# Optimization experiments

Hardware: AMD Instinct MI355X
Metric: run time of the kernel (lower is better)

## Reference

```python
import jax, jax.numpy as jnp
import numpy as np
from jax import lax

A_RATIOS = (0.5, 1.0, 2.0)
A_SCALES = (8, 16, 32)
FEAT_STRIDE = 16
BASE_SIZE = 16
PRE_NMS = 6000     # n_test_pre_nms
POST_NMS = 300     # n_test_post_nms
NMS_THRESH = 0.7
MIN_SIZE = 16.0
SCALE = 1.0        # forward(scale=1.0) default
NEG = -1e10


def _anchor_base():
    # standard generate_anchor_base: centered at (8,8), ratios x scales
    py = px = BASE_SIZE / 2.0
    rows = []
    for r in A_RATIOS:
        for s in A_SCALES:
            h = BASE_SIZE * s * np.sqrt(r)
            w = BASE_SIZE * s * np.sqrt(1.0 / r)
            rows.append([py - h / 2.0, px - w / 2.0, py + h / 2.0, px + w / 2.0])
    return np.asarray(rows, np.float32)  # (A, 4)


def _all_anchors(height, width):
    base = jnp.asarray(_anchor_base())                                  # (A, 4)
    sy = (jnp.arange(height) * FEAT_STRIDE).astype(jnp.float32)
    sx = (jnp.arange(width) * FEAT_STRIDE).astype(jnp.float32)
    gy, gx = jnp.meshgrid(sy, sx, indexing='ij')
    shift = jnp.stack([gy.ravel(), gx.ravel(), gy.ravel(), gx.ravel()], axis=1)  # (K, 4)
    anch = base[None, :, :] + shift[:, None, :]                         # (K, A, 4)
    return anch.reshape(-1, 4)                                          # (K*A, 4)


def _conv(x, w, b, pad):
    y = lax.conv_general_dilated(x, w, (1, 1), [(pad, pad), (pad, pad)],
                                 dimension_numbers=('NCHW', 'OIHW', 'NCHW'))
    return y + b[None, :, None, None]


def _loc2bbox(anchors, locs):
    h = anchors[:, 2] - anchors[:, 0]
    w = anchors[:, 3] - anchors[:, 1]
    cy = anchors[:, 0] + 0.5 * h
    cx = anchors[:, 1] + 0.5 * w
    dy, dx, dh, dw = locs[:, 0], locs[:, 1], locs[:, 2], locs[:, 3]
    ncy = dy * h + cy
    ncx = dx * w + cx
    nh = jnp.exp(dh) * h
    nw = jnp.exp(dw) * w
    return jnp.stack([ncy - 0.5 * nh, ncx - 0.5 * nw,
                      ncy + 0.5 * nh, ncx + 0.5 * nw], axis=1)


def _iou_one_vs_all(box, boxes):
    ty = jnp.maximum(box[0], boxes[:, 0])
    tx = jnp.maximum(box[1], boxes[:, 1])
    by = jnp.minimum(box[2], boxes[:, 2])
    bx = jnp.minimum(box[3], boxes[:, 3])
    inter = jnp.maximum(by - ty, 0.0) * jnp.maximum(bx - tx, 0.0)
    a1 = (box[2] - box[0]) * (box[3] - box[1])
    a2 = (boxes[:, 2] - boxes[:, 0]) * (boxes[:, 3] - boxes[:, 1])
    return inter / (a1 + a2 - inter + 1e-9)


def _nms(boxes, scores):
    # greedy NMS with fixed POST_NMS output; invalid slots are zero boxes
    def step(s, _):
        i = jnp.argmax(s)
        valid = s[i] > NEG / 2
        ious = _iou_one_vs_all(boxes[i], boxes)
        s = jnp.where(ious > NMS_THRESH, NEG, s)  # suppresses self (iou=1)
        return s, (i, valid)
    _, (idx, valid) = lax.scan(step, scores, None, length=POST_NMS)
    return boxes[idx] * valid[:, None].astype(boxes.dtype)  # (POST_NMS, 4)


def _proposals(anchors, locs, fg, img_h, img_w):
    boxes = _loc2bbox(anchors, locs)
    boxes = jnp.stack([jnp.clip(boxes[:, 0], 0.0, img_h),
                       jnp.clip(boxes[:, 1], 0.0, img_w),
                       jnp.clip(boxes[:, 2], 0.0, img_h),
                       jnp.clip(boxes[:, 3], 0.0, img_w)], axis=1)
    hs = boxes[:, 2] - boxes[:, 0]
    ws = boxes[:, 3] - boxes[:, 1]
    ok = (hs >= MIN_SIZE * SCALE) & (ws >= MIN_SIZE * SCALE)
    sc = jnp.where(ok, fg, NEG)
    top_sc, idx = lax.top_k(sc, PRE_NMS)
    return _nms(boxes[idx], top_sc)


def reference(base_feat, W_conv1, b_conv1, W_score, b_score, W_loc, b_loc, img_h, img_w):
    N, _, H, W = base_feat.shape
    A = 9
    mid = jax.nn.relu(_conv(base_feat, W_conv1, b_conv1, 1))            # (N,512,H,W)
    rpn_locs = _conv(mid, W_loc, b_loc, 0).transpose(0, 2, 3, 1).reshape(N, H * W * A, 4)
    raw = _conv(mid, W_score, b_score, 0).transpose(0, 2, 3, 1)          # (N,H,W,2A)
    rpn_scores = raw.reshape(N, H * W * A, 2)
    fg = jax.nn.softmax(raw.reshape(N, H, W, A, 2), axis=-1)[..., 1].reshape(N, -1)
    anchors = _all_anchors(H, W)                                         # (H*W*A,4)
    ih, iw = float(img_h), float(img_w)
    prop = jax.vmap(lambda l, f: _proposals(anchors, l, f, ih, iw))(rpn_locs, fg)
    rois = prop.reshape(N * POST_NMS, 4)
    roi_indices = jnp.repeat(jnp.arange(N, dtype=jnp.int32), POST_NMS)
    return rpn_locs, rpn_scores, rois, roi_indices, anchors


def setup_inputs() -> dict:
    key = jax.random.key(0)
    k0, k1, k2, k3 = jax.random.split(key, 4)
    N, C, H, W = 4, 512, 64, 64
    nA = 9
    return {
        'base_feat': jax.random.normal(k0, (N, C, H, W), jnp.float32),
        'W_conv1': 0.01 * jax.random.normal(k1, (512, 512, 3, 3), jnp.float32),
        'b_conv1': jnp.zeros((512,), jnp.float32),
        'W_score': 0.01 * jax.random.normal(k2, (2 * nA, 512, 1, 1), jnp.float32),
        'b_score': jnp.zeros((2 * nA,), jnp.float32),
        'W_loc': 0.01 * jax.random.normal(k3, (4 * nA, 512, 1, 1), jnp.float32),
        'b_loc': jnp.zeros((4 * nA,), jnp.float32),
        'img_h': 1024,
        'img_w': 1024,
    }
```

## Files before the change

kernel.cpp:

```cpp
#include <hip/hip_runtime.h>
#include <math.h>

#define HH 64
#define WW 64
#define NIMG 4
#define CIN 512
#define AA 9
#define HWA (HH*WW*AA)
#define PRE_NMS 6000
#define POST_NMS 300
#define NEGV (-1e10f)
#define NEGK 0xD01502F9u
#define NWORD 94

#define OFF1 589824
#define OFF2 884736
#define OFF3 889536
#define OFF4 890736

typedef unsigned int u32;
typedef unsigned long long u64;
typedef _Float16 f16;
typedef _Float16 half8 __attribute__((ext_vector_type(8)));
typedef float f32x4 __attribute__((ext_vector_type(4)));

__device__ __forceinline__ void gload_lds16(const void* g, void* l)
{
    __builtin_amdgcn_global_load_lds((const __attribute__((address_space(1))) void*)g,
                                     (__attribute__((address_space(3))) void*)l,
                                     16, 0, 0);
}

__global__ __launch_bounds__(256) void k_prep_x(const float* __restrict__ x,
                                                f16* __restrict__ xh,
                                                f16* __restrict__ xl)
{
    __shared__ float tile[64][65];
    int ci0 = blockIdx.x * 64, y = blockIdx.y, n = blockIdx.z;
    int t = threadIdx.x;
    #pragma unroll
    for (int l = 0; l < 16; ++l) {
        int idx = l * 256 + t;
        int cc = idx >> 6, xc = idx & 63;
        tile[cc][xc] = x[((size_t)(n * CIN + ci0 + cc) * HH + y) * WW + xc];
    }
    __syncthreads();
    #pragma unroll
    for (int l = 0; l < 16; ++l) {
        int idx = l * 256 + t;
        int xc = idx >> 6, cc = idx & 63;
        float v = tile[cc][xc];
        f16 hi = (f16)v;
        f16 lo = (f16)(v - (float)hi);
        size_t o = ((size_t)(n * 64 + y) * 64 + xc) * 512 + ci0 + cc;
        xh[o] = hi; xl[o] = lo;
    }
}

__global__ __launch_bounds__(256) void k_prep_w(const float* __restrict__ W1,
                                                f16* __restrict__ wh,
                                                f16* __restrict__ wl)
{
    int idx = blockIdx.x * 256 + threadIdx.x;
    int co = idx >> 9, ci = idx & 511;
    #pragma unroll
    for (int tap = 0; tap < 9; ++tap) {
        float v = W1[(size_t)idx * 9 + tap];
        f16 hi = (f16)v;
        f16 lo = (f16)(v - (float)hi);
        size_t o = ((size_t)tap * 512 + co) * 512 + ci;
        wh[o] = hi; wl[o] = lo;
    }
}

__global__ __launch_bounds__(256, 4) void k_conv_mfma(const f16* __restrict__ xh,
                                                      const f16* __restrict__ xl,
                                                      const f16* __restrict__ wh,
                                                      const f16* __restrict__ wl,
                                                      const float* __restrict__ bias,
                                                      float* __restrict__ mid)
{
    __shared__ f16 sX[2][4][64][32];
    const int t = threadIdx.x;
    const int lid = blockIdx.x + 8 * (blockIdx.y + 32 * blockIdx.z);
    const int logical = (lid & 7) * 128 + (lid >> 3);
    const int co0 = (logical & 7) * 64;
    const int g = logical >> 3;
    const int yb = g & 31, n = g >> 5;
    const int y0 = yb * 2;
    const int wv = t >> 6, lane = t & 63;
    const int q = lane >> 4, li = lane & 15;
    const int mh = wv & 1;
    const int xhp = wv >> 1;

    if (yb == 0 || yb == 31) {
        int rowu = (yb == 0) ? 0 : 3072;
        u32* p = (u32*)&sX[0][0][0][0];
        #pragma unroll
        for (int l = 0; l < 8; ++l) {
            int idx = l * 256 + t;
            int plane = idx >> 10, r = idx & 1023;
            p[plane * 4096 + rowu + r] = 0;
        }
    }

    f32x4 acc[2][2][2];
    #pragma unroll
    for (int mt = 0; mt < 2; ++mt)
        #pragma unroll
        for (int xn = 0; xn < 2; ++xn)
            #pragma unroll
            for (int yy = 0; yy < 2; ++yy)
                acc[mt][xn][yy] = (f32x4){0.f, 0.f, 0.f, 0.f};

    auto prefetch = [&](int ci0) {
        #pragma unroll
        for (int m = 0; m < 8; ++m) {
            int k2 = wv * 8 + m;
            int plane = k2 >> 4;
            int row = (k2 >> 2) & 3;
            int gy = y0 - 1 + row;
            if ((unsigned)gy < 64u) {
                int col = ((k2 & 3) << 4) + (lane >> 2);
                int s = (lane & 3) ^ ((lane >> 3) & 3);
                const f16* src = (plane ? xl : xh) +
                    (((size_t)(n * 64 + gy) * 64 + col) * 512 + ci0 + s * 8);
                f16* dst = &sX[0][0][0][0] + (size_t)k2 * 512 + lane * 8;
                gload_lds16(src, dst);
            }
        }
    };

    const size_t wb0 = (size_t)(co0 + mh * 32 + li) * 512 + q * 8;
    const f16* pWh = wh + wb0;
    const f16* pWl = wl + wb0;
    half8 wa[2][2], wn[2][2];
    auto loadW = [&](half8 (&w)[2][2], int ci0, int tap) {
        #pragma unroll
        for (int mt = 0; mt < 2; ++mt) {
            size_t off = (size_t)tap * 262144 + (size_t)mt * 8192 + ci0;
            w[0][mt] = *(const half8*)(pWh + off);
            w[1][mt] = *(const half8*)(pWl + off);
        }
    };

    const f16* pB[2][3];
    bool ob[2][3];
    #pragma unroll
    for (int xn = 0; xn < 2; ++xn)
        #pragma unroll
        for (int kx = 0; kx < 3; ++kx) {
            int xc = xhp * 32 + xn * 16 + li;
            int colr = xc + kx - 1;
            bool o = (colr < 0) || (colr > 63);
            int colc = o ? 0 : colr;
            int qe = q ^ ((colc >> 1) & 3);
            ob[xn][kx] = o;
            pB[xn][kx] = &sX[0][0][colc][qe * 8];
        }

    const half8 zero8 = {(f16)0, (f16)0, (f16)0, (f16)0, (f16)0, (f16)0, (f16)0, (f16)0};

    auto loadB = [&](half8 (&Bf)[2][2][2], int tap) {
        const int ky = tap / 3, kx = tap - ky * 3;
        #pragma unroll
        for (int xn = 0; xn < 2; ++xn) {
            const f16* pb = pB[xn][kx];
            #pragma unroll
            for (int yy = 0; yy < 2; ++yy) {
                const f16* ph = pb + (yy + ky) * 2048;
                half8 vh = *(const half8*)ph;
                half8 vl = *(const half8*)(ph + 8192);
                if (ob[xn][kx]) { vh = zero8; vl = zero8; }
                Bf[0][xn][yy] = vh; Bf[1][xn][yy] = vl;
            }
        }
    };

    prefetch(0);
    loadW(wa, 0, 0);

    for (int chunk = 0; chunk < 16; ++chunk) {
        const int ci0 = chunk * 32;
        __syncthreads();

        half8 B0[2][2][2], Bn[2][2][2];
        loadB(B0, 0);

        #pragma unroll
        for (int tap = 0; tap < 9; ++tap) {
            if (tap < 8) {
                loadW(wn, ci0, tap + 1);
                loadB(Bn, tap + 1);
            }
            #pragma unroll
            for (int mt = 0; mt < 2; ++mt)
                #pragma unroll
                for (int xn = 0; xn < 2; ++xn)
                    #pragma unroll
                    for (int yy = 0; yy < 2; ++yy)
                        acc[mt][xn][yy] = __builtin_amdgcn_mfma_f32_16x16x32_f16(wa[0][mt], B0[0][xn][yy], acc[mt][xn][yy], 0, 0, 0);
            #pragma unroll
            for (int mt = 0; mt < 2; ++mt)
                #pragma unroll
                for (int xn = 0; xn < 2; ++xn)
                    #pragma unroll
                    for (int yy = 0; yy < 2; ++yy)
                        acc[mt][xn][yy] = __builtin_amdgcn_mfma_f32_16x16x32_f16(wa[0][mt], B0[1][xn][yy], acc[mt][xn][yy], 0, 0, 0);
            #pragma unroll
            for (int mt = 0; mt < 2; ++mt)
                #pragma unroll
                for (int xn = 0; xn < 2; ++xn)
                    #pragma unroll
                    for (int yy = 0; yy < 2; ++yy)
                        acc[mt][xn][yy] = __builtin_amdgcn_mfma_f32_16x16x32_f16(wa[1][mt], B0[0][xn][yy], acc[mt][xn][yy], 0, 0, 0);

            if (tap < 8) {
                #pragma unroll
                for (int pl = 0; pl < 2; ++pl)
                    #pragma unroll
                    for (int mt = 0; mt < 2; ++mt) wa[pl][mt] = wn[pl][mt];
                #pragma unroll
                for (int pl = 0; pl < 2; ++pl)
                    #pragma unroll
                    for (int xn = 0; xn < 2; ++xn)
                        #pragma unroll
                        for (int yy = 0; yy < 2; ++yy) B0[pl][xn][yy] = Bn[pl][xn][yy];
            }
        }

        if (chunk + 1 < 16) {
            __syncthreads();
            prefetch(ci0 + 32);
            loadW(wa, ci0 + 32, 0);
        }
    }

    #pragma unroll
    for (int mt = 0; mt < 2; ++mt) {
        #pragma unroll
        for (int r = 0; r < 4; ++r) {
            int co = co0 + mh * 32 + mt * 16 + q * 4 + r;
            float bv = bias[co];
            #pragma unroll
            for (int xn = 0; xn < 2; ++xn) {
                int xc = xhp * 32 + xn * 16 + li;
                #pragma unroll
                for (int yy = 0; yy < 2; ++yy) {
                    float v = acc[mt][xn][yy][r] + bv;
                    mid[((size_t)(n * 512 + co) * HH + y0 + yy) * WW + xc] = v > 0.f ? v : 0.f;
                }
            }
        }
    }
}

__global__ __launch_bounds__(256) void k_htrans(const float* __restrict__ Ws,
                                                const float* __restrict__ Wl,
                                                float* __restrict__ Wt2)
{
    int i = blockIdx.x * 256 + threadIdx.x;
    if (i >= 512 * 64) return;
    int ci = i >> 6, co = i & 63;
    float v = 0.f;
    if (co < 18) v = Ws[co * 512 + ci];
    else if (co < 54) v = Wl[(co - 18) * 512 + ci];
    Wt2[i] = v;
}

__global__ __launch_bounds__(256) void k_hgemm(const float* __restrict__ mid,
                                               const float* __restrict__ Wt2,
                                               float* __restrict__ sraw)
{
    __shared__ float sM[32][64];
    __shared__ float sW2[32][64];
    const int t = threadIdx.x;
    const int px0 = blockIdx.x * 64, n = blockIdx.y;
    const int tx = t & 15, ty = t >> 4;

    float acc[4][4];
    #pragma unroll
    for (int c = 0; c < 4; ++c)
        #pragma unroll
        for (int j = 0; j < 4; ++j) acc[c][j] = 0.f;

    for (int ci0 = 0; ci0 < 512; ci0 += 32) {
        __syncthreads();
        #pragma unroll
        for (int l = 0; l < 8; ++l) {
            int i = l * 256 + t;
            int ci = i >> 6, px = i & 63;
            sM[ci][px] = mid[((size_t)n * 512 + ci0 + ci) * 4096 + px0 + px];
            sW2[ci][px] = Wt2[(size_t)(ci0 + ci) * 64 + px];
        }
        __syncthreads();
        #pragma unroll
        for (int ci = 0; ci < 32; ++ci) {
            float mv[4], wv[4];
            #pragma unroll
            for (int j = 0; j < 4; ++j) mv[j] = sM[ci][tx * 4 + j];
            #pragma unroll
            for (int c = 0; c < 4; ++c) wv[c] = sW2[ci][ty * 4 + c];
            #pragma unroll
            for (int c = 0; c < 4; ++c)
                #pragma unroll
                for (int j = 0; j < 4; ++j) acc[c][j] += wv[c] * mv[j];
        }
    }
    #pragma unroll
    for (int c = 0; c < 4; ++c) {
        float4 v = make_float4(acc[c][0], acc[c][1], acc[c][2], acc[c][3]);
        *(float4*)&sraw[((size_t)n * 64 + ty * 4 + c) * 4096 + px0 + tx * 4] = v;
    }
}

__global__ __launch_bounds__(256) void k_decode(const float* __restrict__ sraw,
                                                const float* __restrict__ bsc,
                                                const float* __restrict__ blc,
                                                const int* __restrict__ ph,
                                                const int* __restrict__ pw,
                                                float* __restrict__ out,
                                                float* __restrict__ boxes,
                                                u32* __restrict__ key)
{
    int p = blockIdx.x * 256 + threadIdx.x;
    int n = p >> 12, pi = p & 4095;
    int y = pi >> 6, xq = pi & 63;

    const float* S = sraw + (size_t)n * 64 * 4096 + pi;
    float* o0 = out + (size_t)n * 147456;
    float* o1 = out + OFF1 + (size_t)n * 73728;
    float IHf = (float)(*ph), IWf = (float)(*pw);

    #pragma unroll
    for (int a = 0; a < 9; ++a) {
        float s0 = S[(size_t)(2 * a) * 4096] + bsc[2 * a];
        float s1 = S[(size_t)(2 * a + 1) * 4096] + bsc[2 * a + 1];
        float dy = S[(size_t)(18 + 4 * a) * 4096] + blc[4 * a];
        float dx = S[(size_t)(19 + 4 * a) * 4096] + blc[4 * a + 1];
        float dh = S[(size_t)(20 + 4 * a) * 4096] + blc[4 * a + 2];
        float dw = S[(size_t)(21 + 4 * a) * 4096] + blc[4 * a + 3];

        o1[(pi * 9 + a) * 2 + 0] = s0;
        o1[(pi * 9 + a) * 2 + 1] = s1;
        o0[(pi * 9 + a) * 4 + 0] = dy;
        o0[(pi * 9 + a) * 4 + 1] = dx;
        o0[(pi * 9 + a) * 4 + 2] = dh;
        o0[(pi * 9 + a) * 4 + 3] = dw;

        float mm = fmaxf(s0, s1);
        float e0 = expf(s0 - mm), e1 = expf(s1 - mm);
        float fg = e1 / (e0 + e1);

        int ri = a / 3, si = a - ri * 3;
        double s = (double)(8 << si);
        double rr = (ri == 0) ? 0.5 : ((ri == 1) ? 1.0 : 2.0);
        double hh = 16.0 * s * sqrt(rr);
        double wd = 16.0 * s * sqrt(1.0 / rr);
        float a0 = (float)(8.0 - hh * 0.5) + (float)(y * 16);
        float a1 = (float)(8.0 - wd * 0.5) + (float)(xq * 16);
        float a2 = (float)(8.0 + hh * 0.5) + (float)(y * 16);
        float a3 = (float)(8.0 + wd * 0.5) + (float)(xq * 16);

        float h = a2 - a0, w = a3 - a1;
        float cy = a0 + 0.5f * h, cx = a1 + 0.5f * w;
        float ncy = dy * h + cy, ncx = dx * w + cx;
        float nh = expf(dh) * h, nw = expf(dw) * w;
        float b0 = fminf(fmaxf(ncy - 0.5f * nh, 0.f), IHf);
        float b1 = fminf(fmaxf(ncx - 0.5f * nw, 0.f), IWf);
        float b2 = fminf(fmaxf(ncy + 0.5f * nh, 0.f), IHf);
        float b3 = fminf(fmaxf(ncx + 0.5f * nw, 0.f), IWf);

        bool ok = (b2 - b0 >= 16.0f) && (b3 - b1 >= 16.0f);
        float sc = ok ? fg : NEGV;

        int gi = n * HWA + pi * 9 + a;
        ((float4*)boxes)[gi] = make_float4(b0, b1, b2, b3);
        u32 u = __float_as_uint(sc);
        u32 kasc = (u & 0x80000000u) ? ~u : (u | 0x80000000u);
        key[gi] = ~kasc;
    }
}

__global__ void k_misc(float* __restrict__ out)
{
    int i = blockIdx.x * 256 + threadIdx.x;
    if (i < 4800) out[OFF2 + i] = 0.f;
    if (i < 1200) out[OFF3 + i] = (float)(i / 300);
    if (i < HWA) {
        int pi = i / 9, a = i - pi * 9;
        int y = pi >> 6, xq = pi & 63;
        int ri = a / 3, si = a - ri * 3;
        double s = (double)(8 << si);
        double rr = (ri == 0) ? 0.5 : ((ri == 1) ? 1.0 : 2.0);
        double hh = 16.0 * s * sqrt(rr);
        double wd = 16.0 * s * sqrt(1.0 / rr);
        out[OFF4 + i * 4 + 0] = (float)(8.0 - hh * 0.5) + (float)(y * 16);
        out[OFF4 + i * 4 + 1] = (float)(8.0 - wd * 0.5) + (float)(xq * 16);
        out[OFF4 + i * 4 + 2] = (float)(8.0 + hh * 0.5) + (float)(y * 16);
        out[OFF4 + i * 4 + 3] = (float)(8.0 + wd * 0.5) + (float)(xq * 16);
    }
}

__global__ __launch_bounds__(1024) void k_select(const u32* __restrict__ key,
                                                 u64* __restrict__ cmp,
                                                 int* __restrict__ nvalid)
{
    __shared__ int hist[256];
    __shared__ u32 sPref;
    __shared__ int sR;
    __shared__ int cLess, cEq, cVal;
    int n = blockIdx.x, t = threadIdx.x;
    const u32* k0 = key + (size_t)n * HWA;

    u32 pref = 0, mask = 0;
    int R = PRE_NMS;
    for (int pass = 0; pass < 4; ++pass) {
        int shift = 24 - pass * 8;
        if (t < 256) hist[t] = 0;
        __syncthreads();
        for (int i = t; i < HWA; i += 1024) {
            u32 k = k0[i];
            if ((k & mask) == pref) atomicAdd(&hist[(k >> shift) & 255], 1);
        }
        __syncthreads();
        if (t == 0) {
            int cum = 0;
            for (int b = 0; b < 256; ++b) {
                int c = hist[b];
                if (cum + c >= R) { sPref = pref | ((u32)b << shift); sR = R - cum; break; }
                cum += c;
            }
        }
        __syncthreads();
        pref = sPref; R = sR; mask |= (0xFFu << shift);
        __syncthreads();
    }
    u32 T = pref;
    if (t == 0) { cLess = 0; cEq = 0; cVal = 0; }
    __syncthreads();
    for (int i = t; i < HWA; i += 1024) {
        u32 k = k0[i];
        if (k < NEGK) atomicAdd(&cVal, 1);
        if (k < T) {
            int p = atomicAdd(&cLess, 1);
            cmp[(size_t)n * 8192 + p] = ((u64)k << 32) | (u32)i;
        } else if (k == T) {
            int p = atomicAdd(&cEq, 1);
            if (p < R) cmp[(size_t)n * 8192 + (PRE_NMS - 1 - p)] = ((u64)k << 32) | (u32)i;
        }
    }
    for (int i = PRE_NMS + t; i < 8192; i += 1024) cmp[(size_t)n * 8192 + i] = ~0ull;
    __syncthreads();
    if (t == 0) nvalid[n] = cVal < PRE_NMS ? cVal : PRE_NMS;
}

__global__ __launch_bounds__(1024) void k_sort(const u64* __restrict__ cmp,
                                               const float* __restrict__ boxes,
                                               float* __restrict__ boxesS)
{
    __shared__ u64 sK[8192];
    int n = blockIdx.x, t = threadIdx.x;
    for (int i = t; i < 8192; i += 1024) sK[i] = cmp[(size_t)n * 8192 + i];
    for (unsigned k = 2; k <= 8192; k <<= 1) {
        for (unsigned j = k >> 1; j > 0; j >>= 1) {
            __syncthreads();
            #pragma unroll
            for (int v = 0; v < 8; ++v) {
                int i = v * 1024 + t;
                int ixj = i ^ (int)j;
                if (ixj > i) {
                    u64 a = sK[i], b = sK[ixj];
                    bool up = ((i & (int)k) == 0);
                    if (up ? (a > b) : (a < b)) { sK[i] = b; sK[ixj] = a; }
                }
            }
        }
    }
    __syncthreads();
    const float4* bsrc = (const float4*)boxes + (size_t)n * HWA;
    float4* bdst = (float4*)boxesS + (size_t)n * PRE_NMS;
    for (int i = t; i < PRE_NMS; i += 1024) {
        u32 idx = (u32)(sK[i] & 0xFFFFFFFFu);
        bdst[i] = bsrc[idx];
    }
}

__global__ __launch_bounds__(64) void k_iou(const float* __restrict__ boxesS,
                                            u64* __restrict__ mask)
{
    __shared__ float4 cb[64];
    int w = blockIdx.x, ic = blockIdx.y, n = blockIdx.z;
    if (w < ic) return;
    int t = threadIdx.x;
    const float4* B = (const float4*)boxesS + (size_t)n * PRE_NMS;
    int jc = w * 64 + t;
    cb[t] = (jc < PRE_NMS) ? B[jc] : make_float4(0.f, 0.f, 0.f, 0.f);
    __syncthreads();
    int i = ic * 64 + t;
    if (i >= PRE_NMS) return;
    float4 bb = B[i];
    float area1 = (bb.z - bb.x) * (bb.w - bb.y);
    u64 m = 0;
    #pragma unroll 8
    for (int j = 0; j < 64; ++j) {
        float4 o = cb[j];
        float ty_ = fmaxf(bb.x, o.x), tx_ = fmaxf(bb.y, o.y);
        float by_ = fminf(bb.z, o.z), bx_ = fminf(bb.w, o.w);
        float inter = fmaxf(by_ - ty_, 0.f) * fmaxf(bx_ - tx_, 0.f);
        float area2 = (o.z - o.x) * (o.w - o.y);
        float iou = inter / (area1 + area2 - inter + 1e-9f);
        if (iou > 0.7f) m |= (1ull << j);
    }
    mask[((size_t)n * PRE_NMS + i) * NWORD + w] = m;
}

__global__ __launch_bounds__(64) void k_nms3(const u64* __restrict__ mask,
                                             const int* __restrict__ nvalid,
                                             const float* __restrict__ boxesS,
                                             float* __restrict__ rois)
{
    int n = blockIdx.x, lane = threadIdx.x;
    int nv = nvalid[n];
    const u64* M = mask + (size_t)n * PRE_NMS * NWORD;
    const float4* B = (const float4*)boxesS + (size_t)n * PRE_NMS;

    auto vmask = [&](int w) -> u64 {
        int lo = w * 64;
        if (nv >= lo + 64) return ~0ull;
        if (nv <= lo) return 0ull;
        return (1ull << (nv - lo)) - 1ull;
    };
    u64 vm0 = vmask(lane);
    u64 vm1 = (lane < NWORD - 64) ? vmask(64 + lane) : 0ull;
    u64 rem0 = 0, rem1 = 0;

    int cnt = 0;
    while (cnt < POST_NMS) {
        u64 c0 = (~rem0) & vm0;
        u64 c1 = (~rem1) & vm1;
        int sel;
        u64 b0 = __ballot(c0 != 0);
        if (b0) {
            int l = __builtin_ctzll(b0);
            u64 w = __shfl(c0, l);
            sel = l * 64 + __builtin_ctzll(w);
        } else {
            u64 b1 = __ballot(c1 != 0);
            if (!b1) break;
            int l = __builtin_ctzll(b1);
            u64 w = __shfl(c1, l);
            sel = (64 + l) * 64 + __builtin_ctzll(w);
        }
        if (lane == 0) {
            float4 bb = B[sel];
            float* orow = rois + (size_t)(n * POST_NMS + cnt) * 4;
            orow[0] = bb.x; orow[1] = bb.y; orow[2] = bb.z; orow[3] = bb.w;
        }
        const u64* Mr = M + (size_t)sel * NWORD;
        rem0 |= Mr[lane];
        if (lane < NWORD - 64) rem1 |= Mr[64 + lane];
        cnt++;
    }
}

extern "C" void kernel_launch(void* const* d_in, const int* in_sizes, int n_in,
                              void* d_out, int out_size, void* d_ws, size_t ws_size,
                              hipStream_t stream)
{
    const float* x  = (const float*)d_in[0];
    const float* W1 = (const float*)d_in[1];
    const float* b1 = (const float*)d_in[2];
    const float* Ws = (const float*)d_in[3];
    const float* bs = (const float*)d_in[4];
    const float* Wl = (const float*)d_in[5];
    const float* bl = (const float*)d_in[6];
    const int* ih   = (const int*)d_in[7];
    const int* iw   = (const int*)d_in[8];
    float* out = (float*)d_out;
    char* ws = (char*)d_ws;

    f16*   Wh2    = (f16*)  (ws);
    f16*   Wl2    = (f16*)  (ws + 4718592);
    float* mid    = (float*)(ws + 9437184);
    f16*   xh     = (f16*)  (ws + 42991616);
    f16*   xl     = (f16*)  (ws + 59768832);
    float* boxes  = (float*)(ws + 42991616);
    u32*   key    = (u32*)  (ws + 45350912);
    u64*   cmp    = (u64*)  (ws + 45940736);
    float* boxesS = (float*)(ws + 46202880);
    int*   nval   = (int*)  (ws + 46586880);
    float* Wt2    = (float*)(ws);
    float* sraw   = (float*)(ws + 262144);
    u64*   iomask = (u64*)  (ws + 9437184);

    k_prep_x<<<dim3(8, 64, 4), 256, 0, stream>>>(x, xh, xl);
    k_prep_w<<<1024, 256, 0, stream>>>(W1, Wh2, Wl2);
    k_conv_mfma<<<dim3(8, 32, 4), 256, 0, stream>>>(xh, xl, Wh2, Wl2, b1, mid);
    k_htrans<<<128, 256, 0, stream>>>(Ws, Wl, Wt2);
    k_hgemm<<<dim3(64, 4), 256, 0, stream>>>(mid, Wt2, sraw);
    k_decode<<<64, 256, 0, stream>>>(sraw, bs, bl, ih, iw, out, boxes, key);
    k_misc<<<144, 256, 0, stream>>>(out);
    k_select<<<4, 1024, 0, stream>>>(key, cmp, nval);
    k_sort<<<4, 1024, 0, stream>>>(cmp, boxes, boxesS);
    k_iou<<<dim3(NWORD, NWORD, NIMG), 64, 0, stream>>>(boxesS, iomask);
    k_nms3<<<NIMG, 64, 0, stream>>>(iomask, nval, boxesS, out + OFF2);
}
```

Before: 846.9 us.

## Speed up tail kernels: host anchor table, swizzled register sort, wider IoU, NMS lookahead

Anchor base coordinates are now computed once on the host and passed as a kernel argument, so the per-thread double-precision sqrt math in k_decode and k_misc goes away. The bitonic sort in shared memory uses an XOR-swizzled index to avoid bank conflicts, and it finishes the stages with j<8 inside registers using 8-element compare-exchange networks, which removes many barriers. k_iou now packs four 64-column words per 256-thread block to cut the block count. k_nms3 prefetches the mask row of the next candidate and can emit two boxes per iteration, shortening the serial chain of dependent loads. The sort and NMS changes are the hardest to verify for correctness.

```diff
diff --git a/kernel.cpp b/kernel.cpp
--- a/kernel.cpp
+++ b/kernel.cpp
@@ -23,6 +23,8 @@
 typedef _Float16 f16;
 typedef _Float16 half8 __attribute__((ext_vector_type(8)));
 typedef float f32x4 __attribute__((ext_vector_type(4)));
+
+struct AnchBase { float v[36]; };
 
 __device__ __forceinline__ void gload_lds16(const void* g, void* l)
 {
@@ -321,7 +323,8 @@
                                                 const int* __restrict__ pw,
                                                 float* __restrict__ out,
                                                 float* __restrict__ boxes,
-                                                u32* __restrict__ key)
+                                                u32* __restrict__ key,
+                                                AnchBase ab)
 {
     int p = blockIdx.x * 256 + threadIdx.x;
     int n = p >> 12, pi = p & 4095;
@@ -352,15 +355,10 @@
         float e0 = expf(s0 - mm), e1 = expf(s1 - mm);
         float fg = e1 / (e0 + e1);
 
-        int ri = a / 3, si = a - ri * 3;
-        double s = (double)(8 << si);
-        double rr = (ri == 0) ? 0.5 : ((ri == 1) ? 1.0 : 2.0);
-        double hh = 16.0 * s * sqrt(rr);
-        double wd = 16.0 * s * sqrt(1.0 / rr);
-        float a0 = (float)(8.0 - hh * 0.5) + (float)(y * 16);
-        float a1 = (float)(8.0 - wd * 0.5) + (float)(xq * 16);
-        float a2 = (float)(8.0 + hh * 0.5) + (float)(y * 16);
-        float a3 = (float)(8.0 + wd * 0.5) + (float)(xq * 16);
+        float a0 = ab.v[4 * a + 0] + (float)(y * 16);
+        float a1 = ab.v[4 * a + 1] + (float)(xq * 16);
+        float a2 = ab.v[4 * a + 2] + (float)(y * 16);
+        float a3 = ab.v[4 * a + 3] + (float)(xq * 16);
 
         float h = a2 - a0, w = a3 - a1;
         float cy = a0 + 0.5f * h, cx = a1 + 0.5f * w;
@@ -382,7 +380,7 @@
     }
 }
 
-__global__ void k_misc(float* __restrict__ out)
+__global__ void k_misc(float* __restrict__ out, AnchBase ab)
 {
     int i = blockIdx.x * 256 + threadIdx.x;
     if (i < 4800) out[OFF2 + i] = 0.f;
@@ -390,15 +388,10 @@
     if (i < HWA) {
         int pi = i / 9, a = i - pi * 9;
         int y = pi >> 6, xq = pi & 63;
-        int ri = a / 3, si = a - ri * 3;
-        double s = (double)(8 << si);
-        double rr = (ri == 0) ? 0.5 : ((ri == 1) ? 1.0 : 2.0);
-        double hh = 16.0 * s * sqrt(rr);
-        double wd = 16.0 * s * sqrt(1.0 / rr);
-        out[OFF4 + i * 4 + 0] = (float)(8.0 - hh * 0.5) + (float)(y * 16);
-        out[OFF4 + i * 4 + 1] = (float)(8.0 - wd * 0.5) + (float)(xq * 16);
-        out[OFF4 + i * 4 + 2] = (float)(8.0 + hh * 0.5) + (float)(y * 16);
-        out[OFF4 + i * 4 + 3] = (float)(8.0 + wd * 0.5) + (float)(xq * 16);
+        out[OFF4 + i * 4 + 0] = ab.v[4 * a + 0] + (float)(y * 16);
+        out[OFF4 + i * 4 + 1] = ab.v[4 * a + 1] + (float)(xq * 16);
+        out[OFF4 + i * 4 + 2] = ab.v[4 * a + 2] + (float)(y * 16);
+        out[OFF4 + i * 4 + 3] = ab.v[4 * a + 3] + (float)(xq * 16);
     }
 }
 
@@ -455,56 +448,89 @@
     if (t == 0) nvalid[n] = cVal < PRE_NMS ? cVal : PRE_NMS;
 }
 
+__device__ __forceinline__ int PHI(int i) { return i ^ (((i >> 3) & 7) << 1); }
+__device__ __forceinline__ void cx(u64& a, u64& b, bool up)
+{
+    bool sw = up ? (a > b) : (a < b);
+    u64 x = a, y = b;
+    a = sw ? y : x;
+    b = sw ? x : y;
+}
+
 __global__ __launch_bounds__(1024) void k_sort(const u64* __restrict__ cmp,
                                                const float* __restrict__ boxes,
                                                float* __restrict__ boxesS)
 {
     __shared__ u64 sK[8192];
     int n = blockIdx.x, t = threadIdx.x;
-    for (int i = t; i < 8192; i += 1024) sK[i] = cmp[(size_t)n * 8192 + i];
+    for (int i = t; i < 8192; i += 1024) sK[PHI(i)] = cmp[(size_t)n * 8192 + i];
+
     for (unsigned k = 2; k <= 8192; k <<= 1) {
-        for (unsigned j = k >> 1; j > 0; j >>= 1) {
+        for (unsigned j = k >> 1; j >= 8; j >>= 1) {
             __syncthreads();
             #pragma unroll
             for (int v = 0; v < 8; ++v) {
                 int i = v * 1024 + t;
                 int ixj = i ^ (int)j;
                 if (ixj > i) {
-                    u64 a = sK[i], b = sK[ixj];
+                    u64 a = sK[PHI(i)], b = sK[PHI(ixj)];
                     bool up = ((i & (int)k) == 0);
-                    if (up ? (a > b) : (a < b)) { sK[i] = b; sK[ixj] = a; }
+                    if (up ? (a > b) : (a < b)) { sK[PHI(i)] = b; sK[PHI(ixj)] = a; }
                 }
             }
         }
-    }
-    __syncthreads();
+        __syncthreads();
+        {
+            int base = t * 8;
+            u64 r[8];
+            #pragma unroll
+            for (int e = 0; e < 8; ++e) r[e] = sK[PHI(base + e)];
+            if (k >= 8) {
+                bool up = ((base & (int)k) == 0);
+                cx(r[0], r[4], up); cx(r[1], r[5], up); cx(r[2], r[6], up); cx(r[3], r[7], up);
+                cx(r[0], r[2], up); cx(r[1], r[3], up); cx(r[4], r[6], up); cx(r[5], r[7], up);
+                cx(r[0], r[1], up); cx(r[2], r[3], up); cx(r[4], r[5], up); cx(r[6], r[7], up);
+            } else if (k == 4) {
+                cx(r[0], r[2], true); cx(r[1], r[3], true); cx(r[4], r[6], false); cx(r[5], r[7], false);
+                cx(r[0], r[1], true); cx(r[2], r[3], true); cx(r[4], r[5], false); cx(r[6], r[7], false);
+            } else {
+                cx(r[0], r[1], true); cx(r[2], r[3], false); cx(r[4], r[5], true); cx(r[6], r[7], false);
+            }
+            #pragma unroll
+            for (int e = 0; e < 8; ++e) sK[PHI(base + e)] = r[e];
+        }
+        __syncthreads();
+    }
     const float4* bsrc = (const float4*)boxes + (size_t)n * HWA;
     float4* bdst = (float4*)boxesS + (size_t)n * PRE_NMS;
     for (int i = t; i < PRE_NMS; i += 1024) {
-        u32 idx = (u32)(sK[i] & 0xFFFFFFFFu);
+        u32 idx = (u32)(sK[PHI(i)] & 0xFFFFFFFFu);
         bdst[i] = bsrc[idx];
     }
 }
 
-__global__ __launch_bounds__(64) void k_iou(const float* __restrict__ boxesS,
-                                            u64* __restrict__ mask)
-{
-    __shared__ float4 cb[64];
-    int w = blockIdx.x, ic = blockIdx.y, n = blockIdx.z;
-    if (w < ic) return;
+__global__ __launch_bounds__(256) void k_iou(const float* __restrict__ boxesS,
+                                             u64* __restrict__ mask)
+{
+    int wq = blockIdx.x, ic = blockIdx.y, n = blockIdx.z;
+    if (wq * 4 + 3 < ic) return;
     int t = threadIdx.x;
+    int g = t >> 6, lane = t & 63;
+    int w = wq * 4 + g;
+    __shared__ float4 cb[4][64];
     const float4* B = (const float4*)boxesS + (size_t)n * PRE_NMS;
-    int jc = w * 64 + t;
-    cb[t] = (jc < PRE_NMS) ? B[jc] : make_float4(0.f, 0.f, 0.f, 0.f);
+    int jc = w * 64 + lane;
+    cb[g][lane] = (jc < PRE_NMS) ? B[jc] : make_float4(0.f, 0.f, 0.f, 0.f);
     __syncthreads();
-    int i = ic * 64 + t;
+    int i = ic * 64 + lane;
     if (i >= PRE_NMS) return;
+    if (w >= NWORD || w < ic) return;
     float4 bb = B[i];
     float area1 = (bb.z - bb.x) * (bb.w - bb.y);
     u64 m = 0;
     #pragma unroll 8
     for (int j = 0; j < 64; ++j) {
-        float4 o = cb[j];
+        float4 o = cb[g][j];
         float ty_ = fmaxf(bb.x, o.x), tx_ = fmaxf(bb.y, o.y);
         float by_ = fminf(bb.z, o.z), bx_ = fminf(bb.w, o.w);
         float inter = fmaxf(by_ - ty_, 0.f) * fmaxf(bx_ - tx_, 0.f);
@@ -531,36 +557,62 @@
         if (nv <= lo) return 0ull;
         return (1ull << (nv - lo)) - 1ull;
     };
-    u64 vm0 = vmask(lane);
-    u64 vm1 = (lane < NWORD - 64) ? vmask(64 + lane) : 0ull;
-    u64 rem0 = 0, rem1 = 0;
-
-    int cnt = 0;
-    while (cnt < POST_NMS) {
-        u64 c0 = (~rem0) & vm0;
-        u64 c1 = (~rem1) & vm1;
-        int sel;
-        u64 b0 = __ballot(c0 != 0);
+    u64 c0 = vmask(lane);
+    u64 c1 = (lane < NWORD - 64) ? vmask(64 + lane) : 0ull;
+
+    auto firstbit = [&](u64 a0, u64 a1) -> int {
+        u64 b0 = __ballot(a0 != 0);
         if (b0) {
             int l = __builtin_ctzll(b0);
-            u64 w = __shfl(c0, l);
-            sel = l * 64 + __builtin_ctzll(w);
-        } else {
-            u64 b1 = __ballot(c1 != 0);
-            if (!b1) break;
-            int l = __builtin_ctzll(b1);
-            u64 w = __shfl(c1, l);
-            sel = (64 + l) * 64 + __builtin_ctzll(w);
-        }
+            u64 w = __shfl(a0, l);
+            return l * 64 + __builtin_ctzll(w);
+        }
+        u64 b1 = __ballot(a1 != 0);
+        if (!b1) return -1;
+        int l = __builtin_ctzll(b1);
+        u64 w = __shfl(a1, l);
+        return (64 + l) * 64 + __builtin_ctzll(w);
+    };
+    auto clearbit = [&](u64& a0, u64& a1, int s) {
+        int ws = s >> 6, b = s & 63;
+        if (lane == ws) a0 &= ~(1ull << b);
+        if (lane + 64 == ws) a1 &= ~(1ull << b);
+    };
+    auto emit = [&](int s, int c) {
         if (lane == 0) {
-            float4 bb = B[sel];
-            float* orow = rois + (size_t)(n * POST_NMS + cnt) * 4;
+            float4 bb = B[s];
+            float* orow = rois + (size_t)(n * POST_NMS + c) * 4;
             orow[0] = bb.x; orow[1] = bb.y; orow[2] = bb.z; orow[3] = bb.w;
         }
+    };
+
+    int cnt = 0;
+    int sel = firstbit(c0, c1);
+    while (sel >= 0 && cnt < POST_NMS) {
         const u64* Mr = M + (size_t)sel * NWORD;
-        rem0 |= Mr[lane];
-        if (lane < NWORD - 64) rem1 |= Mr[64 + lane];
-        cnt++;
+        u64 m0 = Mr[lane];
+        u64 m1 = (lane < NWORD - 64) ? Mr[64 + lane] : 0ull;
+
+        u64 d0 = c0, d1 = c1;
+        clearbit(d0, d1, sel);
+        int pred = firstbit(d0, d1);
+        u64 p0 = 0, p1 = 0;
+        if (pred >= 0) {
+            const u64* Pr = M + (size_t)pred * NWORD;
+            p0 = Pr[lane];
+            p1 = (lane < NWORD - 64) ? Pr[64 + lane] : 0ull;
+        }
+
+        emit(sel, cnt); cnt++;
+        c0 = d0 & ~m0; c1 = d1 & ~m1;
+        int nxt = firstbit(c0, c1);
+        if (nxt >= 0 && nxt == pred && cnt < POST_NMS) {
+            emit(pred, cnt); cnt++;
+            clearbit(c0, c1, pred);
+            c0 &= ~p0; c1 &= ~p1;
+            nxt = firstbit(c0, c1);
+        }
+        sel = nxt;
     }
 }
 
@@ -594,15 +646,28 @@
     float* sraw   = (float*)(ws + 262144);
     u64*   iomask = (u64*)  (ws + 9437184);
 
+    AnchBase ab;
+    for (int a = 0; a < 9; ++a) {
+        int ri = a / 3, si = a - ri * 3;
+        double s = (double)(8 << si);
+        double rr = (ri == 0) ? 0.5 : ((ri == 1) ? 1.0 : 2.0);
+        double hh = 16.0 * s * sqrt(rr);
+        double wd = 16.0 * s * sqrt(1.0 / rr);
+        ab.v[a * 4 + 0] = (float)(8.0 - hh * 0.5);
+        ab.v[a * 4 + 1] = (float)(8.0 - wd * 0.5);
+        ab.v[a * 4 + 2] = (float)(8.0 + hh * 0.5);
+        ab.v[a * 4 + 3] = (float)(8.0 + wd * 0.5);
+    }
+
     k_prep_x<<<dim3(8, 64, 4), 256, 0, stream>>>(x, xh, xl);
     k_prep_w<<<1024, 256, 0, stream>>>(W1, Wh2, Wl2);
     k_conv_mfma<<<dim3(8, 32, 4), 256, 0, stream>>>(xh, xl, Wh2, Wl2, b1, mid);
     k_htrans<<<128, 256, 0, stream>>>(Ws, Wl, Wt2);
     k_hgemm<<<dim3(64, 4), 256, 0, stream>>>(mid, Wt2, sraw);
-    k_decode<<<64, 256, 0, stream>>>(sraw, bs, bl, ih, iw, out, boxes, key);
-    k_misc<<<144, 256, 0, stream>>>(out);
+    k_decode<<<64, 256, 0, stream>>>(sraw, bs, bl, ih, iw, out, boxes, key, ab);
+    k_misc<<<144, 256, 0, stream>>>(out, ab);
     k_select<<<4, 1024, 0, stream>>>(key, cmp, nval);
     k_sort<<<4, 1024, 0, stream>>>(cmp, boxes, boxesS);
-    k_iou<<<dim3(NWORD, NWORD, NIMG), 64, 0, stream>>>(boxesS, iomask);
+    k_iou<<<dim3(24, NWORD, NIMG), 256, 0, stream>>>(boxesS, iomask);
     k_nms3<<<NIMG, 64, 0, stream>>>(iomask, nval, boxesS, out + OFF2);
 }
```

Result: slower. 872.6 us (+3.0%).
